# Kernel optimization log

Hardware: AMD Instinct MI355X
Metric: run time of the kernel (lower is better)

Reference implementation:

```python
import jax, jax.numpy as jnp
import numpy as np

N_NODES = 100000
N_EDGES = 1600000
D = 128


def setup_inputs() -> dict:
    key = jax.random.key(0)
    k1, k2, k3 = jax.random.split(key, 3)
    x = jax.random.normal(k1, (N_NODES, D), dtype=jnp.float32)
    W = jax.random.normal(k2, (D, D), dtype=jnp.float32) * (1.0 / np.sqrt(D))
    b = jnp.zeros((D,), dtype=jnp.float32)
    edge_index = jax.random.randint(k3, (2, N_EDGES), 0, N_NODES, dtype=jnp.int64)
    return {"x": x, "W": W, "b": b, "edge_index": edge_index}


def reference(x, W, b, edge_index):
    # GCNBlock: out = relu(GCNConv(x, edge_index)) + x ; returns (out, edge_index)
    # GCNConv (PyG default): add self-loops, symmetric deg^{-1/2} normalization.
    N = x.shape[0]
    h = x @ W  # [N, D] dense transform before aggregation

    loop = jnp.arange(N, dtype=edge_index.dtype)
    src = jnp.concatenate([edge_index[0], loop])  # [E+N]
    dst = jnp.concatenate([edge_index[1], loop])  # [E+N]

    deg = jax.ops.segment_sum(jnp.ones_like(dst, dtype=h.dtype), dst, num_segments=N)
    inv_sqrt = jax.lax.rsqrt(deg)  # deg >= 1 thanks to self-loops
    coef = inv_sqrt[src] * inv_sqrt[dst]  # [E+N]

    # gather messages, scale, scatter-add to destinations
    msg = h[src] * coef[:, None]  # [E+N, D] -- dominant memory traffic
    agg = jax.ops.segment_sum(msg, dst, num_segments=N) + b  # [N, D]

    out = jax.nn.relu(agg) + x  # relu + residual fusion
    return (out, edge_index)
```

## Files before the change

kernel.cpp:

```cpp
#include <hip/hip_runtime.h>


#define DD 128
#define EPB 2048
#define BSH 9
typedef __attribute__((ext_vector_type(8))) short bf16x8;
typedef __attribute__((ext_vector_type(4))) float f32x4;
typedef __attribute__((ext_vector_type(2))) float f32x2;

#if __has_builtin(__builtin_amdgcn_cvt_pk_fp8_f32) && __has_builtin(__builtin_amdgcn_cvt_pk_f32_fp8)
#define FP8PATH 1
#else
#define FP8PATH 0
#endif

__device__ __forceinline__ ushort f2bf(float f) {
    unsigned u = __float_as_uint(f);
    unsigned r = (u + 0x7fffu + ((u >> 16) & 1u)) >> 16;
    return (ushort)r;
}
__device__ __forceinline__ float bflo(unsigned u) { return __uint_as_float(u << 16); }
__device__ __forceinline__ float bfhi(unsigned u) { return __uint_as_float(u & 0xffff0000u); }

__device__ __forceinline__ int ld_src(const int* p, int e, int E, int is64) {
    return is64 ? p[2 * e] : p[e];
}
__device__ __forceinline__ int ld_dst(const int* p, int e, int E, int is64) {
    return is64 ? p[2 * (E + e)] : p[E + e];
}

__device__ __forceinline__ int detect64(const int* __restrict__ p, int E) {
    int lane = threadIdx.x & 63;
    int idx = 2 * lane + 1;
    if (idx >= 2 * E) idx = 2 * E - 1;
    unsigned long long m = __ballot(p[idx] != 0);
    return m == 0ull ? 1 : 0;
}

__global__ __launch_bounds__(256) void kA1(const int* __restrict__ ei, int E, int NB, int nA,
                                           float* __restrict__ outTail, int* __restrict__ H,
                                           const float* __restrict__ W, ushort* __restrict__ Wt) {
    int t = threadIdx.x, a = blockIdx.x;
    if (a >= nA) {
        int i = (a - nA) * 256 + t;
        if (i < DD * DD) {
            int c = i >> 7, k = i & 127;
            Wt[i] = f2bf(W[k * DD + c]);
        }
        return;
    }
    __shared__ int hist[256];
    int is64 = detect64(ei, E);
    if (t < NB) hist[t] = 0;
    __syncthreads();
    int base = a * EPB;
    #pragma unroll
    for (int it = 0; it < EPB / 256; ++it) {
        int e = base + it * 256 + t;
        if (e < E) {
            int s = ld_src(ei, e, E, is64);
            int d = ld_dst(ei, e, E, is64);
            outTail[e] = (float)s;
            outTail[E + e] = (float)d;
            atomicAdd(&hist[d >> BSH], 1);
        }
    }
    __syncthreads();
    if (t < NB) H[a * NB + t] = hist[t];
}

__global__ __launch_bounds__(256) void k_scanH1(int* __restrict__ H, int nA, int NB,
                                                int* __restrict__ colsum) {
    __shared__ int s[256];
    int b = blockIdx.x, t = threadIdx.x;
    int K = (nA + 255) / 256;
    int base = t * K;
    int local = 0;
    for (int j = 0; j < K; ++j) {
        int a = base + j;
        if (a < nA) local += H[a * NB + b];
    }
    s[t] = local;
    __syncthreads();
    #pragma unroll
    for (int off = 1; off < 256; off <<= 1) {
        int u = (t >= off) ? s[t - off] : 0;
        __syncthreads();
        s[t] += u;
        __syncthreads();
    }
    int run = s[t] - local;
    for (int j = 0; j < K; ++j) {
        int a = base + j;
        if (a < nA) { int v = H[a * NB + b]; H[a * NB + b] = run; run += v; }
    }
    if (t == 255) colsum[b] = s[255];
}

__global__ __launch_bounds__(256) void kA2(const int* __restrict__ ei, int E, int NB,
                                           const int* __restrict__ H,
                                           const int* __restrict__ colsum,
                                           unsigned* __restrict__ brec) {
    __shared__ int bs[256];
    __shared__ int cur[256];
    int t = threadIdx.x, a = blockIdx.x;
    int is64 = detect64(ei, E);
    int v = (t < NB) ? colsum[t] : 0;
    bs[t] = v;
    __syncthreads();
    #pragma unroll
    for (int off = 1; off < 256; off <<= 1) {
        int u = (t >= off) ? bs[t - off] : 0;
        __syncthreads();
        bs[t] += u;
        __syncthreads();
    }
    if (t < NB) cur[t] = H[a * NB + t] + bs[t] - v;
    __syncthreads();
    int base = a * EPB;
    #pragma unroll
    for (int it = 0; it < EPB / 256; ++it) {
        int e = base + it * 256 + t;
        if (e < E) {
            int s = ld_src(ei, e, E, is64);
            int d = ld_dst(ei, e, E, is64);
            int pos = atomicAdd(&cur[d >> BSH], 1);
            brec[pos] = (unsigned)s | ((unsigned)(d & 511) << 17);
        }
    }
}

__global__ __launch_bounds__(512) void kB(const unsigned* __restrict__ brec,
                                          const int* __restrict__ colsum, int NB, int N,
                                          int E, unsigned* __restrict__ recs,
                                          int* __restrict__ rowstart, float* __restrict__ invs) {
    __shared__ int bs[256];
    __shared__ int hist[512];
    __shared__ int scn[512];
    __shared__ int cur[512];
    int b = blockIdx.x, t = threadIdx.x;
    if (t < 256) bs[t] = (t < NB) ? colsum[t] : 0;
    __syncthreads();
    #pragma unroll
    for (int off = 1; off < 256; off <<= 1) {
        int u = 0;
        if (t < 256 && t >= off) u = bs[t - off];
        __syncthreads();
        if (t < 256) bs[t] += u;
        __syncthreads();
    }
    int cs = colsum[b];
    int hi = bs[b];
    int lo = hi - cs;
    hist[t] = 0;
    __syncthreads();
    for (int i = lo + t; i < hi; i += 512) atomicAdd(&hist[brec[i] >> 17], 1);
    __syncthreads();
    int hv = hist[t];
    scn[t] = hv;
    __syncthreads();
    #pragma unroll
    for (int off = 1; off < 512; off <<= 1) {
        int u = (t >= off) ? scn[t - off] : 0;
        __syncthreads();
        scn[t] += u;
        __syncthreads();
    }
    int excl = scn[t] - hv;
    int node = (b << BSH) + t;
    if (node < N) {
        rowstart[node] = lo + excl;
        invs[node] = rsqrtf((float)(1 + hv));
    }
    cur[t] = lo + excl;
    if (b == NB - 1 && t == 0) rowstart[N] = E;
    __syncthreads();
    for (int i = lo + t; i < hi; i += 512) {
        unsigned r = brec[i];
        int pos = atomicAdd(&cur[r >> 17], 1);
        recs[pos] = r & 0x1FFFFu;
    }
}

__global__ __launch_bounds__(256) void k_gemm_h(const float* __restrict__ x,
                                                const ushort* __restrict__ Wt,
                                                const float* __restrict__ invs,
                                                unsigned* __restrict__ hs, int N) {
    int wave = threadIdx.x >> 6, lane = threadIdx.x & 63;
    int rowBase = blockIdx.x * 64 + wave * 16;
    int rfrag = lane & 15, kgrp = lane >> 4;
    f32x4 zero = {0.f, 0.f, 0.f, 0.f};
    f32x4 acc[8];
    #pragma unroll
    for (int n = 0; n < 8; ++n) acc[n] = zero;

    int arow = rowBase + rfrag;
    bool av = arow < N;
    const float* xrow = x + (size_t)(av ? arow : 0) * DD + kgrp * 8;
    const ushort* wbase = Wt + rfrag * DD + kgrp * 8;

    #pragma unroll
    for (int ks = 0; ks < 4; ++ks) {
        bf16x8 bnode = {0, 0, 0, 0, 0, 0, 0, 0};
        if (av) {
            float4 f0 = *(const float4*)(xrow + ks * 32);
            float4 f1 = *(const float4*)(xrow + ks * 32 + 4);
            bnode[0] = (short)f2bf(f0.x); bnode[1] = (short)f2bf(f0.y);
            bnode[2] = (short)f2bf(f0.z); bnode[3] = (short)f2bf(f0.w);
            bnode[4] = (short)f2bf(f1.x); bnode[5] = (short)f2bf(f1.y);
            bnode[6] = (short)f2bf(f1.z); bnode[7] = (short)f2bf(f1.w);
        }
        #pragma unroll
        for (int n = 0; n < 8; ++n) {
            bf16x8 aw = *(const bf16x8*)(wbase + n * 16 * DD + ks * 32);
            acc[n] = __builtin_amdgcn_mfma_f32_16x16x32_bf16(aw, bnode, acc[n], 0, 0, 0);
        }
    }

    int node = rowBase + rfrag;
    if (node < N) {
        float wn = invs[node];
        int csub = kgrp * 4;
#if FP8PATH
        #pragma unroll
        for (int n = 0; n < 8; ++n) {
            int c0 = n * 16 + csub;
            int u = __builtin_amdgcn_cvt_pk_fp8_f32(wn * acc[n][0], wn * acc[n][1], 0, false);
            u = __builtin_amdgcn_cvt_pk_fp8_f32(wn * acc[n][2], wn * acc[n][3], u, true);
            hs[(size_t)node * 32 + (c0 >> 2)] = (unsigned)u;
        }
#else
        #pragma unroll
        for (int n = 0; n < 8; ++n) {
            int c0 = n * 16 + csub;
            uint2 u;
            u.x = (unsigned)f2bf(wn * acc[n][0]) | ((unsigned)f2bf(wn * acc[n][1]) << 16);
            u.y = (unsigned)f2bf(wn * acc[n][2]) | ((unsigned)f2bf(wn * acc[n][3]) << 16);
            *(uint2*)&hs[(size_t)node * 64 + (c0 >> 1)] = u;
        }
#endif
    }
}

#if FP8PATH
__device__ __forceinline__ void agg_batch16_fp8(const ushort* h16, const unsigned* recs,
                                                int e, int lane, float& ax, float& ay) {
    unsigned sv[16]; ushort vv[16];
    #pragma unroll
    for (int j = 0; j < 16; ++j) sv[j] = recs[e + j];
    #pragma unroll
    for (int j = 0; j < 16; ++j) vv[j] = h16[(size_t)sv[j] * 64 + lane];
    #pragma unroll
    for (int j = 0; j < 16; ++j) {
        f32x2 f = __builtin_amdgcn_cvt_pk_f32_fp8((int)(unsigned)vv[j], false);
        ax += f.x; ay += f.y;
    }
}
__device__ __forceinline__ void agg_batch8_fp8(const ushort* h16, const unsigned* recs,
                                               int e, int lane, float& ax, float& ay) {
    unsigned sv[8]; ushort vv[8];
    #pragma unroll
    for (int j = 0; j < 8; ++j) sv[j] = recs[e + j];
    #pragma unroll
    for (int j = 0; j < 8; ++j) vv[j] = h16[(size_t)sv[j] * 64 + lane];
    #pragma unroll
    for (int j = 0; j < 8; ++j) {
        f32x2 f = __builtin_amdgcn_cvt_pk_f32_fp8((int)(unsigned)vv[j], false);
        ax += f.x; ay += f.y;
    }
}
#endif

__global__ __launch_bounds__(256) void k_agg_out(const unsigned* __restrict__ hs,
                                                 const int* __restrict__ rowstart,
                                                 const float* __restrict__ invs,
                                                 const unsigned* __restrict__ recs,
                                                 const float* __restrict__ bb,
                                                 const float* __restrict__ x,
                                                 float* __restrict__ out, int N) {
    int wave = threadIdx.x >> 6, lane = threadIdx.x & 63;
#if FP8PATH
    int nodeA = blockIdx.x * 8 + wave * 2;
    if (nodeA >= N) return;
    int nodeB = nodeA + 1;
    bool hasB = nodeB < N;
    const ushort* h16 = (const ushort*)hs;
    float axA, ayA, axB = 0.f, ayB = 0.f;
    {
        f32x2 f = __builtin_amdgcn_cvt_pk_f32_fp8((int)(unsigned)h16[(size_t)nodeA * 64 + lane], false);
        axA = f.x; ayA = f.y;
    }
    int eA = rowstart[nodeA], eA1 = rowstart[nodeA + 1];
    int eB = eA1, eB1 = eA1;
    if (hasB) {
        f32x2 f = __builtin_amdgcn_cvt_pk_f32_fp8((int)(unsigned)h16[(size_t)nodeB * 64 + lane], false);
        axB = f.x; ayB = f.y;
        eB1 = rowstart[nodeB + 1];
    }
    while (eA + 8 <= eA1 && eB + 8 <= eB1) {
        unsigned svA[8], svB[8]; ushort vvA[8], vvB[8];
        #pragma unroll
        for (int j = 0; j < 8; ++j) svA[j] = recs[eA + j];
        #pragma unroll
        for (int j = 0; j < 8; ++j) svB[j] = recs[eB + j];
        #pragma unroll
        for (int j = 0; j < 8; ++j) vvA[j] = h16[(size_t)svA[j] * 64 + lane];
        #pragma unroll
        for (int j = 0; j < 8; ++j) vvB[j] = h16[(size_t)svB[j] * 64 + lane];
        #pragma unroll
        for (int j = 0; j < 8; ++j) {
            f32x2 f = __builtin_amdgcn_cvt_pk_f32_fp8((int)(unsigned)vvA[j], false);
            axA += f.x; ayA += f.y;
        }
        #pragma unroll
        for (int j = 0; j < 8; ++j) {
            f32x2 f = __builtin_amdgcn_cvt_pk_f32_fp8((int)(unsigned)vvB[j], false);
            axB += f.x; ayB += f.y;
        }
        eA += 8; eB += 8;
    }
    for (; eA + 16 <= eA1; eA += 16) agg_batch16_fp8(h16, recs, eA, lane, axA, ayA);
    if (eA + 8 <= eA1) { agg_batch8_fp8(h16, recs, eA, lane, axA, ayA); eA += 8; }
    for (; eA < eA1; ++eA) {
        f32x2 f = __builtin_amdgcn_cvt_pk_f32_fp8((int)(unsigned)h16[(size_t)recs[eA] * 64 + lane], false);
        axA += f.x; ayA += f.y;
    }
    for (; eB + 16 <= eB1; eB += 16) agg_batch16_fp8(h16, recs, eB, lane, axB, ayB);
    if (eB + 8 <= eB1) { agg_batch8_fp8(h16, recs, eB, lane, axB, ayB); eB += 8; }
    for (; eB < eB1; ++eB) {
        f32x2 f = __builtin_amdgcn_cvt_pk_f32_fp8((int)(unsigned)h16[(size_t)recs[eB] * 64 + lane], false);
        axB += f.x; ayB += f.y;
    }
    float2 bv = ((const float2*)bb)[lane];
    {
        float wn = invs[nodeA];
        float2 xv = ((const float2*)x)[(size_t)nodeA * 64 + lane];
        float2 o;
        o.x = fmaxf(axA * wn + bv.x, 0.f) + xv.x;
        o.y = fmaxf(ayA * wn + bv.y, 0.f) + xv.y;
        ((float2*)out)[(size_t)nodeA * 64 + lane] = o;
    }
    if (hasB) {
        float wn = invs[nodeB];
        float2 xv = ((const float2*)x)[(size_t)nodeB * 64 + lane];
        float2 o;
        o.x = fmaxf(axB * wn + bv.x, 0.f) + xv.x;
        o.y = fmaxf(ayB * wn + bv.y, 0.f) + xv.y;
        ((float2*)out)[(size_t)nodeB * 64 + lane] = o;
    }
#else
    int base = blockIdx.x * 8 + wave * 2;
    for (int node = base; node < base + 2 && node < N; ++node) {
        float wn = invs[node];
        unsigned us = hs[(size_t)node * 64 + lane];
        float accx = bflo(us), accy = bfhi(us);
        int e = rowstart[node], e1 = rowstart[node + 1];
        for (; e + 8 <= e1; e += 8) {
            unsigned sv[8], vv[8];
            #pragma unroll
            for (int j = 0; j < 8; ++j) sv[j] = recs[e + j];
            #pragma unroll
            for (int j = 0; j < 8; ++j) vv[j] = hs[(size_t)sv[j] * 64 + lane];
            #pragma unroll
            for (int j = 0; j < 8; ++j) { accx += bflo(vv[j]); accy += bfhi(vv[j]); }
        }
        for (; e < e1; ++e) {
            unsigned v0 = hs[(size_t)recs[e] * 64 + lane];
            accx += bflo(v0); accy += bfhi(v0);
        }
        float2 bv = ((const float2*)bb)[lane];
        float2 xv = ((const float2*)x)[(size_t)node * 64 + lane];
        float2 o;
        o.x = fmaxf(accx * wn + bv.x, 0.f) + xv.x;
        o.y = fmaxf(accy * wn + bv.y, 0.f) + xv.y;
        ((float2*)out)[(size_t)node * 64 + lane] = o;
    }
#endif
}

__global__ void k_sniff(const int* __restrict__ p, int n_check, int* __restrict__ flag) {
    __shared__ int any_nonzero;
    if (threadIdx.x == 0) any_nonzero = 0;
    __syncthreads();
    int j = threadIdx.x;
    if (j < n_check && p[2 * j + 1] != 0) any_nonzero = 1;
    __syncthreads();
    if (threadIdx.x == 0) *flag = any_nonzero ? 0 : 1;
}

__global__ void k_count_echo(const int* __restrict__ ei, int E, int* __restrict__ cnt,
                             float* __restrict__ outTail, unsigned* __restrict__ rank,
                             const int* __restrict__ flagp) {
    int is64 = *flagp;
    int e = blockIdx.x * blockDim.x + threadIdx.x;
    if (e < E) {
        int s = ld_src(ei, e, E, is64);
        int d = ld_dst(ei, e, E, is64);
        outTail[e] = (float)s;
        outTail[E + e] = (float)d;
        rank[e] = (unsigned)atomicAdd(&cnt[d], 1);
    }
}

__global__ void k_scan1(const int* __restrict__ cnt, int N, int* __restrict__ rowstart,
                        int* __restrict__ bsum) {
    __shared__ int s[1024];
    int tid = threadIdx.x;
    int i = blockIdx.x * 1024 + tid;
    int v = (i < N) ? cnt[i] : 0;
    s[tid] = v;
    __syncthreads();
    for (int off = 1; off < 1024; off <<= 1) {
        int t2 = (tid >= off) ? s[tid - off] : 0;
        __syncthreads();
        s[tid] += t2;
        __syncthreads();
    }
    if (i < N) rowstart[i] = s[tid] - v;
    if (tid == 1023) bsum[blockIdx.x] = s[1023];
}

__global__ void k_scan2(const int* __restrict__ bsum, int nblk, int* __restrict__ boff) {
    __shared__ int s[128];
    int t = threadIdx.x;
    if (t < nblk) s[t] = bsum[t];
    __syncthreads();
    if (t == 0) {
        int a = 0;
        for (int i = 0; i < nblk; i++) { int v = s[i]; s[i] = a; a += v; }
    }
    __syncthreads();
    if (t < nblk) boff[t] = s[t];
}

__global__ void k_scan3(int N, int E, int* __restrict__ rowstart, const int* __restrict__ boff,
                        const int* __restrict__ cnt, float* __restrict__ invs) {
    int i = blockIdx.x * blockDim.x + threadIdx.x;
    if (i < N) {
        int r = rowstart[i] + boff[i >> 10];
        rowstart[i] = r;
        invs[i] = rsqrtf((float)(1 + cnt[i]));
    }
    if (i == 0 && blockIdx.x == 0) rowstart[N] = E;
}

__global__ void k_fill_r(const int* __restrict__ ei, int E, const int* __restrict__ rowstart,
                         const unsigned* __restrict__ rank, unsigned* __restrict__ recs,
                         const int* __restrict__ flagp) {
    int is64 = *flagp;
    int e = blockIdx.x * blockDim.x + threadIdx.x;
    if (e < E) {
        int d = ld_dst(ei, e, E, is64);
        int s = ld_src(ei, e, E, is64);
        recs[rowstart[d] + rank[e]] = (unsigned)s;
    }
}

__global__ void k_agg_f32(const float* __restrict__ x, const int* __restrict__ rowstart,
                          const float* __restrict__ invs, const unsigned* __restrict__ recs,
                          int N, float* __restrict__ aggOut) {
    int node = blockIdx.x * 4 + (threadIdx.x >> 6);
    int lane = threadIdx.x & 63;
    if (node >= N) return;
    const float2* xr = (const float2*)x;
    float wn = invs[node];
    float2 xself = xr[(size_t)node * 64 + lane];
    float accx = wn * xself.x, accy = wn * xself.y;
    int e = rowstart[node], e1 = rowstart[node + 1];
    for (; e < e1; ++e) {
        unsigned s = recs[e];
        float w = invs[s];
        float2 v = xr[(size_t)s * 64 + lane];
        accx = fmaf(w, v.x, accx); accy = fmaf(w, v.y, accy);
    }
    float2 o; o.x = accx * wn; o.y = accy * wn;
    ((float2*)aggOut)[(size_t)node * 64 + lane] = o;
}

#define GROWS 32
__global__ __launch_bounds__(128) void k_gemm_f32(float* __restrict__ out, const float* __restrict__ Wm,
                                                  const float* __restrict__ bb,
                                                  const float* __restrict__ x, int N) {
    __shared__ float Ws[64 * DD];
    __shared__ float As[DD * GROWS];
    int t = threadIdx.x;
    int rowBase = blockIdx.x * GROWS;
    {
        int r = t & 31, kq = t >> 5;
        if (rowBase + r < N) {
            const float4* Av = (const float4*)(out + (size_t)(rowBase + r) * DD);
            #pragma unroll
            for (int q = 0; q < 8; q++) {
                float4 v = Av[kq * 8 + q];
                int k = (kq * 8 + q) * 4;
                As[(k + 0) * GROWS + r] = v.x;
                As[(k + 1) * GROWS + r] = v.y;
                As[(k + 2) * GROWS + r] = v.z;
                As[(k + 3) * GROWS + r] = v.w;
            }
        } else {
            #pragma unroll
            for (int q = 0; q < 8; q++) {
                int k = (kq * 8 + q) * 4;
                As[(k + 0) * GROWS + r] = 0.f;
                As[(k + 1) * GROWS + r] = 0.f;
                As[(k + 2) * GROWS + r] = 0.f;
                As[(k + 3) * GROWS + r] = 0.f;
            }
        }
    }
    int tx = t & 15, ty = t >> 4;
    int c0 = tx * 8, r0 = ty * 4;
    float acc[4][8];
    #pragma unroll
    for (int i = 0; i < 4; i++)
        #pragma unroll
        for (int j = 0; j < 8; j++) acc[i][j] = 0.f;
    for (int kk = 0; kk < DD; kk += 64) {
        __syncthreads();
        const float4* Wv = (const float4*)(Wm + (size_t)kk * DD);
        #pragma unroll
        for (int i = 0; i < 16; i++) ((float4*)Ws)[t + i * 128] = Wv[t + i * 128];
        __syncthreads();
        #pragma unroll 4
        for (int k = 0; k < 64; k++) {
            const float4 a = *(const float4*)&As[(kk + k) * GROWS + r0];
            const float4 w0 = *(const float4*)&Ws[k * DD + c0];
            const float4 w1 = *(const float4*)&Ws[k * DD + c0 + 4];
            const float av[4] = {a.x, a.y, a.z, a.w};
            const float wv[8] = {w0.x, w0.y, w0.z, w0.w, w1.x, w1.y, w1.z, w1.w};
            #pragma unroll
            for (int i = 0; i < 4; i++)
                #pragma unroll
                for (int j = 0; j < 8; j++) acc[i][j] = fmaf(av[i], wv[j], acc[i][j]);
        }
    }
    float bv[8];
    {
        float4 b0 = *(const float4*)&bb[c0];
        float4 b1 = *(const float4*)&bb[c0 + 4];
        bv[0] = b0.x; bv[1] = b0.y; bv[2] = b0.z; bv[3] = b0.w;
        bv[4] = b1.x; bv[5] = b1.y; bv[6] = b1.z; bv[7] = b1.w;
    }
    #pragma unroll
    for (int i = 0; i < 4; i++) {
        int row = rowBase + r0 + i;
        if (row < N) {
            const float4 xv0 = *(const float4*)&x[(size_t)row * DD + c0];
            const float4 xv1 = *(const float4*)&x[(size_t)row * DD + c0 + 4];
            float4 o0, o1;
            o0.x = fmaxf(acc[i][0] + bv[0], 0.f) + xv0.x;
            o0.y = fmaxf(acc[i][1] + bv[1], 0.f) + xv0.y;
            o0.z = fmaxf(acc[i][2] + bv[2], 0.f) + xv0.z;
            o0.w = fmaxf(acc[i][3] + bv[3], 0.f) + xv0.w;
            o1.x = fmaxf(acc[i][4] + bv[4], 0.f) + xv1.x;
            o1.y = fmaxf(acc[i][5] + bv[5], 0.f) + xv1.y;
            o1.z = fmaxf(acc[i][6] + bv[6], 0.f) + xv1.z;
            o1.w = fmaxf(acc[i][7] + bv[7], 0.f) + xv1.w;
            *(float4*)&out[(size_t)row * DD + c0] = o0;
            *(float4*)&out[(size_t)row * DD + c0 + 4] = o1;
        }
    }
}

extern "C" void kernel_launch(void* const* d_in, const int* in_sizes, int n_in,
                              void* d_out, int out_size, void* d_ws, size_t ws_size,
                              hipStream_t stream) {
    const float* x = (const float*)d_in[0];
    const float* W = (const float*)d_in[1];
    const float* b = (const float*)d_in[2];
    const int*   ei = (const int*)d_in[3];
    int N = in_sizes[0] / DD;
    int E = in_sizes[3] / 2;
    float* out = (float*)d_out;
    float* outTail = out + (size_t)N * DD;

    int NB = (N + 511) >> BSH;
    int nA = (E + EPB - 1) / EPB;

    char* wsb = (char*)d_ws;
    size_t off = 0;
    unsigned* brec = (unsigned*)(wsb + off);  off += (size_t)E * 4;
    unsigned* recs = (unsigned*)(wsb + off);  off += (size_t)E * 4;
    unsigned* hs   = (unsigned*)(wsb + off);  off += (size_t)N * 64 * 4;
    ushort*   Wt   = (ushort*)(wsb + off);    off += (size_t)DD * DD * 2;
    int* H         = (int*)(wsb + off);       off += (size_t)nA * NB * 4;
    int* colsum    = (int*)(wsb + off);       off += (size_t)NB * 4;
    int* rowstart  = (int*)(wsb + off);       off += (size_t)(N + 1) * 4;
    float* invs    = (float*)(wsb + off);     off += (size_t)N * 4;

    bool newpath = (ws_size >= off) && (NB <= 256) && (nA <= 1024) && (N <= 131072) && (E >= 64);

    if (newpath) {
        kA1<<<nA + 64, 256, 0, stream>>>(ei, E, NB, nA, outTail, H, W, Wt);
        k_scanH1<<<NB, 256, 0, stream>>>(H, nA, NB, colsum);
        kA2<<<nA, 256, 0, stream>>>(ei, E, NB, H, colsum, brec);
        kB<<<NB, 512, 0, stream>>>(brec, colsum, NB, N, E, recs, rowstart, invs);
        k_gemm_h<<<(N + 63) / 64, 256, 0, stream>>>(x, Wt, invs, hs, N);
        k_agg_out<<<(N + 7) / 8, 256, 0, stream>>>(hs, rowstart, invs, recs, b, x, out, N);
    } else {
        off = 0;
        unsigned* recsF = (unsigned*)(wsb + off);  off += (size_t)E * 4;
        unsigned* rank  = (unsigned*)(wsb + off);  off += (size_t)E * 4;
        int* cnt        = (int*)(wsb + off);       off += (size_t)N * 4;
        int* rowstartF  = (int*)(wsb + off);       off += (size_t)(N + 1) * 4;
        float* invsF    = (float*)(wsb + off);     off += (size_t)N * 4;
        int* bsum       = (int*)(wsb + off);       off += 512 * 4;
        int* boff       = (int*)(wsb + off);       off += 512 * 4;
        int* flagF      = (int*)(wsb + off);

        hipMemsetAsync(cnt, 0, sizeof(int) * (size_t)N, stream);
        k_sniff<<<1, 1024, 0, stream>>>(ei, 1024, flagF);
        k_count_echo<<<(E + 255) / 256, 256, 0, stream>>>(ei, E, cnt, outTail, rank, flagF);
        int nblk = (N + 1023) / 1024;
        k_scan1<<<nblk, 1024, 0, stream>>>(cnt, N, rowstartF, bsum);
        k_scan2<<<1, 128, 0, stream>>>(bsum, nblk, boff);
        k_scan3<<<(N + 255) / 256, 256, 0, stream>>>(N, E, rowstartF, boff, cnt, invsF);
        k_fill_r<<<(E + 255) / 256, 256, 0, stream>>>(ei, E, rowstartF, rank, recsF, flagF);
        k_agg_f32<<<(N + 3) / 4, 256, 0, stream>>>(x, rowstartF, invsF, recsF, N, out);
        k_gemm_f32<<<(N + GROWS - 1) / GROWS, 128, 0, stream>>>(out, W, b, x, N);
    }
}
```

Baseline: 151.7 us.

## Stage bucket scatter in shared memory for coalesced global writes

The bucket-partition kernel now builds a local histogram, scans it, and places each block's records into a shared-memory buffer grouped by bucket. Each wave then copies contiguous bucket runs to global memory, so writes are contiguous instead of scattered 4-byte stores. In exchange the kernel does an extra 256-entry scan with many syncthreads, holds 8 KB of LDS plus per-thread register arrays, and the per-bucket copy loop is short because buckets average only about 8 records.

```diff
diff --git a/kernel.cpp b/kernel.cpp
--- a/kernel.cpp
+++ b/kernel.cpp
@@ -102,11 +102,18 @@
                                            const int* __restrict__ colsum,
                                            unsigned* __restrict__ brec) {
     __shared__ int bs[256];
-    __shared__ int cur[256];
+    __shared__ int gb[256];
+    __shared__ int lhist[256];
+    __shared__ int lso[256];
+    __shared__ int lcur[256];
+    __shared__ unsigned lrec[EPB];
     int t = threadIdx.x, a = blockIdx.x;
+    int wave = t >> 6, lane = t & 63;
     int is64 = detect64(ei, E);
+
     int v = (t < NB) ? colsum[t] : 0;
     bs[t] = v;
+    lhist[t] = 0;
     __syncthreads();
     #pragma unroll
     for (int off = 1; off < 256; off <<= 1) {
@@ -115,18 +122,54 @@
         bs[t] += u;
         __syncthreads();
     }
-    if (t < NB) cur[t] = H[a * NB + t] + bs[t] - v;
-    __syncthreads();
+    if (t < NB) gb[t] = H[a * NB + t] + bs[t] - v;
+    __syncthreads();
+
     int base = a * EPB;
+    int sreg[EPB / 256], dreg[EPB / 256];
     #pragma unroll
     for (int it = 0; it < EPB / 256; ++it) {
         int e = base + it * 256 + t;
         if (e < E) {
-            int s = ld_src(ei, e, E, is64);
-            int d = ld_dst(ei, e, E, is64);
-            int pos = atomicAdd(&cur[d >> BSH], 1);
-            brec[pos] = (unsigned)s | ((unsigned)(d & 511) << 17);
-        }
+            sreg[it] = ld_src(ei, e, E, is64);
+            dreg[it] = ld_dst(ei, e, E, is64);
+            atomicAdd(&lhist[dreg[it] >> BSH], 1);
+        } else {
+            sreg[it] = -1;
+        }
+    }
+    __syncthreads();
+
+    int hv = lhist[t];
+    lso[t] = hv;
+    __syncthreads();
+    #pragma unroll
+    for (int off = 1; off < 256; off <<= 1) {
+        int u = (t >= off) ? lso[t - off] : 0;
+        __syncthreads();
+        lso[t] += u;
+        __syncthreads();
+    }
+    int excl = lso[t] - hv;
+    lso[t] = excl;
+    lcur[t] = excl;
+    __syncthreads();
+
+    #pragma unroll
+    for (int it = 0; it < EPB / 256; ++it) {
+        if (sreg[it] >= 0) {
+            int d = dreg[it];
+            int pos = atomicAdd(&lcur[d >> BSH], 1);
+            lrec[pos] = (unsigned)sreg[it] | ((unsigned)(d & 511) << 17);
+        }
+    }
+    __syncthreads();
+
+    for (int b = wave; b < NB; b += 4) {
+        int l0 = lso[b], cntb = lhist[b];
+        int g = gb[b];
+        for (int j = lane; j < cntb; j += 64)
+            brec[g + j] = lrec[l0 + j];
     }
 }
 
```

Result: slower. 154.9 us (+2.1%).
